# Performance work log

Hardware: AMD Instinct MI355X
Metric: run time of the kernel (lower is better)

Reference implementation:

```python
import jax, jax.numpy as jnp
from jax import lax
import numpy as np

B = 1024
CH = 32          # decomp.channel
LEVEL = 3        # decomp.level
CTOT = CH * (LEVEL + 1)   # 128, ODE state dim == GRU input dim
T_POINTS = 96    # decomp.eval_time_points
PRED_LEN = 96
HID = 128


def _dopri5_traj(y0, ts, Wo, bo):
    """Fixed-grid Dormand-Prince 5(4) integration of dy/dt = tanh(y Wo^T + bo).
    y0: [B, CTOT]; ts: [T]. Returns trajectory [T, B, CTOT]."""
    f = lambda y: jnp.tanh(y @ Wo.T + bo)

    def step(y, dt):
        k1 = f(y)
        k2 = f(y + dt * (0.2 * k1))
        k3 = f(y + dt * (3.0 / 40 * k1 + 9.0 / 40 * k2))
        k4 = f(y + dt * (44.0 / 45 * k1 - 56.0 / 15 * k2 + 32.0 / 9 * k3))
        k5 = f(y + dt * (19372.0 / 6561 * k1 - 25360.0 / 2187 * k2 + 64448.0 / 6561 * k3 - 212.0 / 729 * k4))
        k6 = f(y + dt * (9017.0 / 3168 * k1 - 355.0 / 33 * k2 + 46732.0 / 5247 * k3 + 49.0 / 176 * k4 - 5103.0 / 18656 * k5))
        y_next = y + dt * (35.0 / 384 * k1 + 500.0 / 1113 * k3 + 125.0 / 192 * k4 - 2187.0 / 6784 * k5 + 11.0 / 84 * k6)
        return y_next, y_next

    _, ys = lax.scan(step, y0, ts[1:] - ts[:-1])
    return jnp.concatenate([y0[None], ys], axis=0)


def _gru_layer(xs, W_ih, W_hh, b_ih, b_hh):
    """PyTorch-semantics GRU layer. xs: [T, B, D] -> hidden states [T, B, H]."""
    gi = jnp.einsum('tbd,gd->tbg', xs, W_ih) + b_ih  # precompute input gates
    H = W_hh.shape[1]

    def cell(h, gi_t):
        gh = h @ W_hh.T + b_hh
        i_r, i_z, i_n = jnp.split(gi_t, 3, axis=-1)
        h_r, h_z, h_n = jnp.split(gh, 3, axis=-1)
        r = jax.nn.sigmoid(i_r + h_r)
        z = jax.nn.sigmoid(i_z + h_z)
        n = jnp.tanh(i_n + r * h_n)
        h_new = (1.0 - z) * n + z * h
        return h_new, h_new

    h0 = jnp.zeros((xs.shape[1], H), xs.dtype)
    _, hs = lax.scan(cell, h0, gi)
    return hs


def setup_inputs() -> dict:
    key = jax.random.key(0)
    ks = jax.random.split(key, 20)
    s = 0.08  # ~1/sqrt(128), keeps GRU/ODE in a stable regime
    return {
        'x': jax.random.normal(ks[0], (B, CH, 256), jnp.float32),
        'yl': jax.random.normal(ks[1], (B, CH, 1), jnp.float32),
        'yh': jax.random.normal(ks[2], (B, CH * LEVEL, 1), jnp.float32),
        'W_ode': jax.random.normal(ks[3], (CTOT, CTOT), jnp.float32) * 0.05,
        'b_ode': jax.random.normal(ks[4], (CTOT,), jnp.float32) * 0.05,
        'W_ih0': jax.random.normal(ks[5], (3 * HID, CTOT), jnp.float32) * s,
        'W_hh0': jax.random.normal(ks[6], (3 * HID, HID), jnp.float32) * s,
        'b_ih0': jax.random.normal(ks[7], (3 * HID,), jnp.float32) * s,
        'b_hh0': jax.random.normal(ks[8], (3 * HID,), jnp.float32) * s,
        'W_ih1': jax.random.normal(ks[9], (3 * HID, HID), jnp.float32) * s,
        'W_hh1': jax.random.normal(ks[10], (3 * HID, HID), jnp.float32) * s,
        'b_ih1': jax.random.normal(ks[11], (3 * HID,), jnp.float32) * s,
        'b_hh1': jax.random.normal(ks[12], (3 * HID,), jnp.float32) * s,
        'W1': jax.random.normal(ks[13], (64, HID), jnp.float32) * s,
        'b1': jax.random.normal(ks[14], (64,), jnp.float32) * s,
        'W2': jax.random.normal(ks[15], (PRED_LEN * CH, 64), jnp.float32) * 0.125,
        'b2': jax.random.normal(ks[16], (PRED_LEN * CH,), jnp.float32) * 0.125,
    }


def reference(x, yl, yh, W_ode, b_ode,
              W_ih0, W_hh0, b_ih0, b_hh0,
              W_ih1, W_hh1, b_ih1, b_hh1,
              W1, b1, W2, b2):
    # coeffs = cat([yl] + yh, dim=1) -> [B, CTOT, 1] -> squeeze coeff length (=1)
    coeffs = jnp.concatenate([yl, yh], axis=1)[..., 0]  # [B, CTOT]
    ts = jnp.linspace(0.0, 1.0, T_POINTS)
    traj = _dopri5_traj(coeffs, ts, W_ode, b_ode)  # [T, B, CTOT]
    # rearrange 't b c l -> b t (c l)' with l == 1; GRU scans over leading T axis
    h1 = _gru_layer(traj, W_ih0, W_hh0, b_ih0, b_hh0)   # [T, B, HID]
    h2 = _gru_layer(h1, W_ih1, W_hh1, b_ih1, b_hh1)     # [T, B, HID]
    last = h2[-1]                                        # [B, HID]
    hidden = jax.nn.gelu(last @ W1.T + b1, approximate=False)
    pred = hidden @ W2.T + b2                            # [B, PRED_LEN*CH]
    return pred.reshape(-1, CH, PRED_LEN)
```

## Files before the change

kernel.cpp:

```cpp
#include <hip/hip_runtime.h>
#include <hip/hip_bf16.h>
#include <math.h>

#define TPTS 96
#define CTOT 128
#define LDP 134

typedef __bf16 bf16x8_t __attribute__((ext_vector_type(8)));
typedef float f32x4_t __attribute__((ext_vector_type(4)));
typedef unsigned short us8_t __attribute__((ext_vector_type(8)));

__device__ __forceinline__ unsigned short f2b(float f) {
    union { float f; unsigned int i; } v; v.f = f;
    unsigned int r = v.i + 0x7fffu + ((v.i >> 16) & 1u);
    return (unsigned short)(r >> 16);
}
__device__ __forceinline__ unsigned int packbf2(float a, float b) {
    return (unsigned int)f2b(a) | ((unsigned int)f2b(b) << 16);
}
__device__ __forceinline__ uint2 pack4(float v0, float v1, float v2, float v3) {
    uint2 w; w.x = packbf2(v0, v1); w.y = packbf2(v2, v3); return w;
}
__device__ __forceinline__ f32x4_t mfma16(bf16x8_t a, bf16x8_t b, f32x4_t c) {
    return __builtin_amdgcn_mfma_f32_16x16x32_bf16(a, b, c, 0, 0, 0);
}
__device__ __forceinline__ bf16x8_t ldfrag(const unsigned short* p) {
    us8_t v = *(const us8_t*)p;
    return __builtin_bit_cast(bf16x8_t, v);
}
__device__ __forceinline__ bf16x8_t ldfragW(const float* p) {
    float4 a = *(const float4*)p;
    float4 b = *(const float4*)(p + 4);
    bf16x8_t r;
    r[0] = __builtin_bit_cast(__bf16, f2b(a.x)); r[1] = __builtin_bit_cast(__bf16, f2b(a.y));
    r[2] = __builtin_bit_cast(__bf16, f2b(a.z)); r[3] = __builtin_bit_cast(__bf16, f2b(a.w));
    r[4] = __builtin_bit_cast(__bf16, f2b(b.x)); r[5] = __builtin_bit_cast(__bf16, f2b(b.y));
    r[6] = __builtin_bit_cast(__bf16, f2b(b.z)); r[7] = __builtin_bit_cast(__bf16, f2b(b.w));
    return r;
}
__device__ __forceinline__ float tanh2(float x) {
    float e = __expf(x + x);
    return 1.f - __fdividef(2.f, e + 1.f);
}
__device__ __forceinline__ float sigm(float x) {
    return __fdividef(1.f, 1.f + __expf(-x));
}

__device__ __forceinline__ void waitflag(unsigned int* f, unsigned int want) {
    if (threadIdx.x == 0) {
        int guard = 0;
        while (__hip_atomic_load(f, __ATOMIC_ACQUIRE, __HIP_MEMORY_SCOPE_AGENT) != want) {
            __builtin_amdgcn_s_sleep(2);
            if (++guard > (1 << 21)) break;
        }
    }
    __syncthreads();
}
__device__ __forceinline__ void setflag(unsigned int* f, unsigned int val) {
    if (threadIdx.x == 0)
        __hip_atomic_store(f, val, __ATOMIC_RELEASE, __HIP_MEMORY_SCOPE_AGENT);
}

__global__ void __launch_bounds__(512, 2)
ode_forecaster(const float* __restrict__ yl,
               const float* __restrict__ yh,
               const float* __restrict__ Wode,
               const float* __restrict__ bode,
               const float* __restrict__ Wih0,
               const float* __restrict__ Whh0,
               const float* __restrict__ bih0,
               const float* __restrict__ bhh0,
               const float* __restrict__ Wih1,
               const float* __restrict__ Whh1,
               const float* __restrict__ bih1,
               const float* __restrict__ bhh1,
               const float* __restrict__ W1v,
               const float* __restrict__ b1v,
               const float* __restrict__ W2v,
               const float* __restrict__ b2v,
               float* __restrict__ outp,
               char* __restrict__ wsb)
{
    const int role = blockIdx.x >> 6;
    const int c    = blockIdx.x & 63;
    const int tid  = threadIdx.x, lane = tid & 63, wv = tid >> 6;
    const int l15  = lane & 15, quad = lane >> 4;
    const int fbase = wv * 16 + quad * 4;
    const int rbase = c * 16;

    __shared__ __align__(16) unsigned short zbuf[2][16][LDP];
    __shared__ __align__(16) unsigned short hidbuf[16][72];

    unsigned short* yTraj  = (unsigned short*)(wsb);
    unsigned short* h1Traj = (unsigned short*)(wsb + 0x2000000);
    unsigned int*   yflag  = (unsigned int*)(wsb + 0x4000000);
    unsigned int*   h1flag = (unsigned int*)(wsb + 0x4010000);
#define YMAGIC(t)  (0x5E000000u + (unsigned)(t))
#define H1MAGIC(t) (0x6E000000u + (unsigned)(t))

    if (role == 0) {
        bf16x8_t wode[4];
#pragma unroll
        for (int kt = 0; kt < 4; ++kt)
            wode[kt] = ldfragW(Wode + (wv * 16 + l15) * CTOT + kt * 32 + quad * 8);
        float bo[4];
        {
            float4 b4 = *(const float4*)(bode + fbase);
            bo[0] = b4.x; bo[1] = b4.y; bo[2] = b4.z; bo[3] = b4.w;
        }
        float y[4];
        {
            int row = rbase + l15;
#pragma unroll
            for (int i = 0; i < 4; ++i) {
                int f = fbase + i;
                y[i] = (f < 32) ? yl[row * 32 + f] : yh[row * 96 + (f - 32)];
            }
            uint2 pk = pack4(y[0], y[1], y[2], y[3]);
            *(uint2*)&zbuf[0][l15][fbase] = pk;
            *(uint2*)(yTraj + ((size_t)row) * CTOT + fbase) = pk;
        }
        __syncthreads();
        setflag(&yflag[c * 128 + 0], YMAGIC(0));

        const float dt = 1.0f / 95.0f;
        const float d10 = dt * 0.2f;
        const float d20 = dt * (3.f/40.f),  d21 = dt * (9.f/40.f);
        const float d30 = dt * (44.f/45.f), d31 = dt * (-56.f/15.f), d32 = dt * (32.f/9.f);
        const float d40 = dt * (19372.f/6561.f), d41 = dt * (-25360.f/2187.f),
                    d42 = dt * (64448.f/6561.f), d43 = dt * (-212.f/729.f);
        const float d50 = dt * (9017.f/3168.f), d51 = dt * (-355.f/33.f),
                    d52 = dt * (46732.f/5247.f), d53 = dt * (49.f/176.f),
                    d54 = dt * (-5103.f/18656.f);
        const float e0 = dt * (35.f/384.f), e2 = dt * (500.f/1113.f), e3 = dt * (125.f/192.f),
                    e4 = dt * (-2187.f/6784.f), e5 = dt * (11.f/84.f);

        int p = 0;
        float kr[6][4];
#pragma unroll 1
        for (int t = 0; t < 95; ++t) {
#pragma unroll
            for (int s = 0; s < 6; ++s) {
                bf16x8_t bf[4];
#pragma unroll
                for (int kt = 0; kt < 4; ++kt)
                    bf[kt] = ldfrag(&zbuf[p][l15][kt * 32 + quad * 8]);
                f32x4_t a0 = {0.f, 0.f, 0.f, 0.f}, a1 = {0.f, 0.f, 0.f, 0.f};
                a0 = mfma16(wode[0], bf[0], a0);
                a1 = mfma16(wode[1], bf[1], a1);
                a0 = mfma16(wode[2], bf[2], a0);
                a1 = mfma16(wode[3], bf[3], a1);
                f32x4_t acc = a0 + a1;
#pragma unroll
                for (int i = 0; i < 4; ++i) kr[s][i] = tanh2(acc[i] + bo[i]);

                if (s < 5) {
                    float z[4];
#pragma unroll
                    for (int i = 0; i < 4; ++i) {
                        float zv;
                        if (s == 0)      zv = y[i] + d10 * kr[0][i];
                        else if (s == 1) zv = y[i] + d20 * kr[0][i] + d21 * kr[1][i];
                        else if (s == 2) zv = y[i] + d30 * kr[0][i] + d31 * kr[1][i] + d32 * kr[2][i];
                        else if (s == 3) zv = y[i] + d40 * kr[0][i] + d41 * kr[1][i]
                                             + d42 * kr[2][i] + d43 * kr[3][i];
                        else             zv = y[i] + d50 * kr[0][i] + d51 * kr[1][i]
                                             + d52 * kr[2][i] + d53 * kr[3][i] + d54 * kr[4][i];
                        z[i] = zv;
                    }
                    *(uint2*)&zbuf[p ^ 1][l15][fbase] = pack4(z[0], z[1], z[2], z[3]);
                } else {
#pragma unroll
                    for (int i = 0; i < 4; ++i)
                        y[i] += e0*kr[0][i] + e2*kr[2][i] + e3*kr[3][i] + e4*kr[4][i] + e5*kr[5][i];
                    uint2 pk = pack4(y[0], y[1], y[2], y[3]);
                    *(uint2*)&zbuf[p ^ 1][l15][fbase] = pk;
                    *(uint2*)(yTraj + ((size_t)(t + 1) * 1024 + rbase + l15) * CTOT + fbase) = pk;
                }
                __syncthreads();
                p ^= 1;
                if (s == 5) setflag(&yflag[c * 128 + t + 1], YMAGIC(t + 1));
            }
        }
        return;
    }

    const float* Wih = (role == 1) ? Wih0 : Wih1;
    const float* Whh = (role == 1) ? Whh0 : Whh1;
    const float* bih = (role == 1) ? bih0 : bih1;
    const float* bhh = (role == 1) ? bhh0 : bhh1;
    const unsigned short* src = (role == 1) ? yTraj : h1Traj;
    unsigned int* sflag = (role == 1) ? yflag : h1flag;

    bf16x8_t wih[3][4], whh[3][4];
#pragma unroll
    for (int g = 0; g < 3; ++g)
#pragma unroll
        for (int kt = 0; kt < 4; ++kt) {
            wih[g][kt] = ldfragW(Wih + (size_t)(g * 128 + wv * 16 + l15) * CTOT + kt * 32 + quad * 8);
            whh[g][kt] = ldfragW(Whh + (size_t)(g * 128 + wv * 16 + l15) * CTOT + kt * 32 + quad * 8);
        }
    float br[4], bz[4], bin_[4], bhn[4];
    {
        float4 a0 = *(const float4*)(bih + 0 * 128 + fbase);
        float4 b0 = *(const float4*)(bhh + 0 * 128 + fbase);
        float4 a1 = *(const float4*)(bih + 1 * 128 + fbase);
        float4 b1 = *(const float4*)(bhh + 1 * 128 + fbase);
        float4 a2 = *(const float4*)(bih + 2 * 128 + fbase);
        float4 b2 = *(const float4*)(bhh + 2 * 128 + fbase);
        br[0] = a0.x + b0.x; br[1] = a0.y + b0.y; br[2] = a0.z + b0.z; br[3] = a0.w + b0.w;
        bz[0] = a1.x + b1.x; bz[1] = a1.y + b1.y; bz[2] = a1.z + b1.z; bz[3] = a1.w + b1.w;
        bin_[0] = a2.x; bin_[1] = a2.y; bin_[2] = a2.z; bin_[3] = a2.w;
        bhn[0] = b2.x; bhn[1] = b2.y; bhn[2] = b2.z; bhn[3] = b2.w;
    }

    float h[4] = {0.f, 0.f, 0.f, 0.f};
    *(uint2*)&zbuf[0][l15][fbase] = pack4(0.f, 0.f, 0.f, 0.f);
    int p = 0;
    __syncthreads();

#pragma unroll 1
    for (int t = 0; t < TPTS; ++t) {
        waitflag(&sflag[c * 128 + t], (role == 1) ? YMAGIC(t) : H1MAGIC(t));
        const unsigned short* xp = src + ((size_t)t * 1024 + rbase + l15) * CTOT;
        bf16x8_t ax[4], ah[4];
#pragma unroll
        for (int kt = 0; kt < 4; ++kt) {
            ax[kt] = ldfrag(xp + kt * 32 + quad * 8);
            ah[kt] = ldfrag(&zbuf[p][l15][kt * 32 + quad * 8]);
        }
        f32x4_t gx[3], gh[3];
#pragma unroll
        for (int g = 0; g < 3; ++g) {
            gx[g] = (f32x4_t){0.f, 0.f, 0.f, 0.f};
            gh[g] = (f32x4_t){0.f, 0.f, 0.f, 0.f};
        }
#pragma unroll
        for (int kt = 0; kt < 4; ++kt) {
            gx[0] = mfma16(wih[0][kt], ax[kt], gx[0]);
            gx[1] = mfma16(wih[1][kt], ax[kt], gx[1]);
            gx[2] = mfma16(wih[2][kt], ax[kt], gx[2]);
            gh[0] = mfma16(whh[0][kt], ah[kt], gh[0]);
            gh[1] = mfma16(whh[1][kt], ah[kt], gh[1]);
            gh[2] = mfma16(whh[2][kt], ah[kt], gh[2]);
        }
#pragma unroll
        for (int i = 0; i < 4; ++i) {
            float rr = sigm(gx[0][i] + gh[0][i] + br[i]);
            float zz = sigm(gx[1][i] + gh[1][i] + bz[i]);
            float nn = tanh2((gx[2][i] + bin_[i]) + rr * (gh[2][i] + bhn[i]));
            h[i] = nn + zz * (h[i] - nn);
        }
        uint2 pk = pack4(h[0], h[1], h[2], h[3]);
        *(uint2*)&zbuf[p ^ 1][l15][fbase] = pk;
        if (role == 1)
            *(uint2*)(h1Traj + ((size_t)t * 1024 + rbase + l15) * CTOT + fbase) = pk;
        __syncthreads();
        if (role == 1) setflag(&h1flag[c * 128 + t], H1MAGIC(t));
        p ^= 1;
    }
    if (role == 1) return;

    if (wv < 4) {
        bf16x8_t wf[4], hf[4];
#pragma unroll
        for (int kt = 0; kt < 4; ++kt) {
            wf[kt] = ldfragW(W1v + (size_t)(wv * 16 + l15) * CTOT + kt * 32 + quad * 8);
            hf[kt] = ldfrag(&zbuf[p][l15][kt * 32 + quad * 8]);
        }
        f32x4_t acc = {0.f, 0.f, 0.f, 0.f};
#pragma unroll
        for (int kt = 0; kt < 4; ++kt) acc = mfma16(wf[kt], hf[kt], acc);
        float4 bb = *(const float4*)(b1v + wv * 16 + quad * 4);
        const float* bbp = (const float*)&bb;
        float gl[4];
#pragma unroll
        for (int i = 0; i < 4; ++i) {
            float x = acc[i] + bbp[i];
            gl[i] = 0.5f * x * (1.0f + erff(x * 0.70710678118654752f));
        }
        *(uint2*)&hidbuf[l15][wv * 16 + quad * 4] = pack4(gl[0], gl[1], gl[2], gl[3]);
    }
    __syncthreads();

    bf16x8_t ahid[2];
#pragma unroll
    for (int kt = 0; kt < 2; ++kt)
        ahid[kt] = ldfrag(&hidbuf[l15][kt * 32 + quad * 8]);
#pragma unroll 1
    for (int j = 0; j < 24; ++j) {
        int mt2 = wv * 24 + j;
        bf16x8_t wf0 = ldfragW(W2v + (size_t)(mt2 * 16 + l15) * 64 + quad * 8);
        bf16x8_t wf1 = ldfragW(W2v + (size_t)(mt2 * 16 + l15) * 64 + 32 + quad * 8);
        float4 bv = *(const float4*)(b2v + mt2 * 16 + quad * 4);
        const float* bvp = (const float*)&bv;
        f32x4_t acc = {0.f, 0.f, 0.f, 0.f};
        acc = mfma16(wf0, ahid[0], acc);
        acc = mfma16(wf1, ahid[1], acc);
        float4 o;
        o.x = acc[0] + bvp[0]; o.y = acc[1] + bvp[1];
        o.z = acc[2] + bvp[2]; o.w = acc[3] + bvp[3];
        *(float4*)(outp + (size_t)(rbase + l15) * 3072 + mt2 * 16 + quad * 4) = o;
    }
#undef YMAGIC
#undef H1MAGIC
}

extern "C" void kernel_launch(void* const* d_in, const int* in_sizes, int n_in,
                              void* d_out, int out_size, void* d_ws, size_t ws_size,
                              hipStream_t stream) {
    const float* yl   = (const float*)d_in[1];
    const float* yh   = (const float*)d_in[2];
    const float* Wode = (const float*)d_in[3];
    const float* bode = (const float*)d_in[4];
    const float* Wih0 = (const float*)d_in[5];
    const float* Whh0 = (const float*)d_in[6];
    const float* bih0 = (const float*)d_in[7];
    const float* bhh0 = (const float*)d_in[8];
    const float* Wih1 = (const float*)d_in[9];
    const float* Whh1 = (const float*)d_in[10];
    const float* bih1 = (const float*)d_in[11];
    const float* bhh1 = (const float*)d_in[12];
    const float* W1v  = (const float*)d_in[13];
    const float* b1v  = (const float*)d_in[14];
    const float* W2v  = (const float*)d_in[15];
    const float* b2v  = (const float*)d_in[16];

    ode_forecaster<<<dim3(192), dim3(512), 0, stream>>>(
        yl, yh, Wode, bode, Wih0, Whh0, bih0, bhh0,
        Wih1, Whh1, bih1, bhh1, W1v, b1v, W2v, b2v,
        (float*)d_out, (char*)d_ws);
}
```

Baseline: 798.2 us.

## Add dedicated communication wave for cross-block trajectory handoff with system-scope flags

Adds a ninth wavefront per block that copies each finished 16-row tile from LDS to the global trajectory buffer with system-scope relaxed atomic stores, drains the stores, then sets the ready flag. Compute waves no longer issue global stores or flag releases. Flag waits switch to relaxed system-scope loads with a shorter sleep. It also replaces the exp-based tanh with a clamped rational approximation and uses a hardware packed bf16 convert, trading some accuracy and relying on vmcnt draining rather than release semantics for ordering.

```diff
diff --git a/kernel.cpp b/kernel.cpp
--- a/kernel.cpp
+++ b/kernel.cpp
@@ -5,6 +5,7 @@
 #define TPTS 96
 #define CTOT 128
 #define LDP 134
+#define NTHR 576
 
 typedef __bf16 bf16x8_t __attribute__((ext_vector_type(8)));
 typedef float f32x4_t __attribute__((ext_vector_type(4)));
@@ -16,7 +17,13 @@
     return (unsigned short)(r >> 16);
 }
 __device__ __forceinline__ unsigned int packbf2(float a, float b) {
+#if __has_builtin(__builtin_amdgcn_cvt_pk_bf16_f32)
+    typedef __bf16 bf16x2_t __attribute__((ext_vector_type(2)));
+    bf16x2_t v = __builtin_amdgcn_cvt_pk_bf16_f32(a, b);
+    return __builtin_bit_cast(unsigned int, v);
+#else
     return (unsigned int)f2b(a) | ((unsigned int)f2b(b) << 16);
+#endif
 }
 __device__ __forceinline__ uint2 pack4(float v0, float v1, float v2, float v3) {
     uint2 w; w.x = packbf2(v0, v1); w.y = packbf2(v2, v3); return w;
@@ -38,30 +45,46 @@
     r[6] = __builtin_bit_cast(__bf16, f2b(b.z)); r[7] = __builtin_bit_cast(__bf16, f2b(b.w));
     return r;
 }
-__device__ __forceinline__ float tanh2(float x) {
-    float e = __expf(x + x);
-    return 1.f - __fdividef(2.f, e + 1.f);
+__device__ __forceinline__ float tanhp(float x) {
+    float xc = fminf(fmaxf(x, -4.5f), 4.5f);
+    float t = xc * xc;
+    float n = xc * (135135.f + t * (17325.f + t * (378.f + t)));
+    float d = 135135.f + t * (62370.f + t * (3150.f + 28.f * t));
+    return n * __frcp_rn(d);
 }
 __device__ __forceinline__ float sigm(float x) {
     return __fdividef(1.f, 1.f + __expf(-x));
 }
 
-__device__ __forceinline__ void waitflag(unsigned int* f, unsigned int want) {
+__device__ __forceinline__ void setflag_sys(unsigned int* f, unsigned int val) {
+    __hip_atomic_store(f, val, __ATOMIC_RELAXED, __HIP_MEMORY_SCOPE_SYSTEM);
+}
+__device__ __forceinline__ void waitflag_sys(unsigned int* f, unsigned int want) {
     if (threadIdx.x == 0) {
         int guard = 0;
-        while (__hip_atomic_load(f, __ATOMIC_ACQUIRE, __HIP_MEMORY_SCOPE_AGENT) != want) {
-            __builtin_amdgcn_s_sleep(2);
-            if (++guard > (1 << 21)) break;
+        while (__hip_atomic_load(f, __ATOMIC_RELAXED, __HIP_MEMORY_SCOPE_SYSTEM) != want) {
+            __builtin_amdgcn_s_sleep(1);
+            if (++guard > (1 << 22)) break;
         }
     }
     __syncthreads();
 }
-__device__ __forceinline__ void setflag(unsigned int* f, unsigned int val) {
-    if (threadIdx.x == 0)
-        __hip_atomic_store(f, val, __ATOMIC_RELEASE, __HIP_MEMORY_SCOPE_AGENT);
-}
-
-__global__ void __launch_bounds__(512, 2)
+__device__ __forceinline__ void dma_rows16(const unsigned short zb[16][LDP],
+                                           unsigned long long* dst, int lane) {
+    const int quad = lane >> 4, l15 = lane & 15;
+#pragma unroll
+    for (int i = 0; i < 4; ++i) {
+        int row = i * 4 + quad;
+        us8_t v = *(const us8_t*)&zb[row][l15 * 8];
+        union { us8_t v; unsigned long long q[2]; } u; u.v = v;
+        size_t idx = (size_t)row * 32 + l15 * 2;
+        __hip_atomic_store(dst + idx,     u.q[0], __ATOMIC_RELAXED, __HIP_MEMORY_SCOPE_SYSTEM);
+        __hip_atomic_store(dst + idx + 1, u.q[1], __ATOMIC_RELAXED, __HIP_MEMORY_SCOPE_SYSTEM);
+    }
+}
+#define DRAIN() asm volatile("s_waitcnt vmcnt(0)" ::: "memory")
+
+__global__ void __launch_bounds__(NTHR, 1)
 ode_forecaster(const float* __restrict__ yl,
                const float* __restrict__ yh,
                const float* __restrict__ Wode,
@@ -85,7 +108,7 @@
     const int c    = blockIdx.x & 63;
     const int tid  = threadIdx.x, lane = tid & 63, wv = tid >> 6;
     const int l15  = lane & 15, quad = lane >> 4;
-    const int fbase = wv * 16 + quad * 4;
+    const int fbase = (wv & 7) * 16 + quad * 4;
     const int rbase = c * 16;
 
     __shared__ __align__(16) unsigned short zbuf[2][16][LDP];
@@ -100,28 +123,27 @@
 
     if (role == 0) {
         bf16x8_t wode[4];
-#pragma unroll
-        for (int kt = 0; kt < 4; ++kt)
-            wode[kt] = ldfragW(Wode + (wv * 16 + l15) * CTOT + kt * 32 + quad * 8);
-        float bo[4];
-        {
+        float bo[4], y[4], kr[6][4];
+        if (wv < 8) {
+#pragma unroll
+            for (int kt = 0; kt < 4; ++kt)
+                wode[kt] = ldfragW(Wode + (wv * 16 + l15) * CTOT + kt * 32 + quad * 8);
             float4 b4 = *(const float4*)(bode + fbase);
             bo[0] = b4.x; bo[1] = b4.y; bo[2] = b4.z; bo[3] = b4.w;
-        }
-        float y[4];
-        {
             int row = rbase + l15;
 #pragma unroll
             for (int i = 0; i < 4; ++i) {
                 int f = fbase + i;
                 y[i] = (f < 32) ? yl[row * 32 + f] : yh[row * 96 + (f - 32)];
             }
-            uint2 pk = pack4(y[0], y[1], y[2], y[3]);
-            *(uint2*)&zbuf[0][l15][fbase] = pk;
-            *(uint2*)(yTraj + ((size_t)row) * CTOT + fbase) = pk;
+            *(uint2*)&zbuf[0][l15][fbase] = pack4(y[0], y[1], y[2], y[3]);
         }
         __syncthreads();
-        setflag(&yflag[c * 128 + 0], YMAGIC(0));
+        if (wv == 8) {
+            dma_rows16(zbuf[0], (unsigned long long*)(yTraj + (size_t)rbase * CTOT), lane);
+            DRAIN();
+            setflag_sys(&yflag[c * 128 + 0], YMAGIC(0));
+        }
 
         const float dt = 1.0f / 95.0f;
         const float d10 = dt * 0.2f;
@@ -136,50 +158,55 @@
                     e4 = dt * (-2187.f/6784.f), e5 = dt * (11.f/84.f);
 
         int p = 0;
-        float kr[6][4];
 #pragma unroll 1
         for (int t = 0; t < 95; ++t) {
 #pragma unroll
             for (int s = 0; s < 6; ++s) {
-                bf16x8_t bf[4];
-#pragma unroll
-                for (int kt = 0; kt < 4; ++kt)
-                    bf[kt] = ldfrag(&zbuf[p][l15][kt * 32 + quad * 8]);
-                f32x4_t a0 = {0.f, 0.f, 0.f, 0.f}, a1 = {0.f, 0.f, 0.f, 0.f};
-                a0 = mfma16(wode[0], bf[0], a0);
-                a1 = mfma16(wode[1], bf[1], a1);
-                a0 = mfma16(wode[2], bf[2], a0);
-                a1 = mfma16(wode[3], bf[3], a1);
-                f32x4_t acc = a0 + a1;
-#pragma unroll
-                for (int i = 0; i < 4; ++i) kr[s][i] = tanh2(acc[i] + bo[i]);
-
-                if (s < 5) {
-                    float z[4];
-#pragma unroll
-                    for (int i = 0; i < 4; ++i) {
-                        float zv;
-                        if (s == 0)      zv = y[i] + d10 * kr[0][i];
-                        else if (s == 1) zv = y[i] + d20 * kr[0][i] + d21 * kr[1][i];
-                        else if (s == 2) zv = y[i] + d30 * kr[0][i] + d31 * kr[1][i] + d32 * kr[2][i];
-                        else if (s == 3) zv = y[i] + d40 * kr[0][i] + d41 * kr[1][i]
-                                             + d42 * kr[2][i] + d43 * kr[3][i];
-                        else             zv = y[i] + d50 * kr[0][i] + d51 * kr[1][i]
-                                             + d52 * kr[2][i] + d53 * kr[3][i] + d54 * kr[4][i];
-                        z[i] = zv;
+                if (wv < 8) {
+                    bf16x8_t bf[4];
+#pragma unroll
+                    for (int kt = 0; kt < 4; ++kt)
+                        bf[kt] = ldfrag(&zbuf[p][l15][kt * 32 + quad * 8]);
+                    f32x4_t a0 = {0.f, 0.f, 0.f, 0.f}, a1 = {0.f, 0.f, 0.f, 0.f};
+                    a0 = mfma16(wode[0], bf[0], a0);
+                    a1 = mfma16(wode[1], bf[1], a1);
+                    a0 = mfma16(wode[2], bf[2], a0);
+                    a1 = mfma16(wode[3], bf[3], a1);
+                    f32x4_t acc = a0 + a1;
+#pragma unroll
+                    for (int i = 0; i < 4; ++i) kr[s][i] = tanhp(acc[i] + bo[i]);
+
+                    if (s < 5) {
+                        float z[4];
+#pragma unroll
+                        for (int i = 0; i < 4; ++i) {
+                            float zv;
+                            if (s == 0)      zv = y[i] + d10 * kr[0][i];
+                            else if (s == 1) zv = y[i] + d20 * kr[0][i] + d21 * kr[1][i];
+                            else if (s == 2) zv = y[i] + d30 * kr[0][i] + d31 * kr[1][i] + d32 * kr[2][i];
+                            else if (s == 3) zv = y[i] + d40 * kr[0][i] + d41 * kr[1][i]
+                                                 + d42 * kr[2][i] + d43 * kr[3][i];
+                            else             zv = y[i] + d50 * kr[0][i] + d51 * kr[1][i]
+                                                 + d52 * kr[2][i] + d53 * kr[3][i] + d54 * kr[4][i];
+                            z[i] = zv;
+                        }
+                        *(uint2*)&zbuf[p ^ 1][l15][fbase] = pack4(z[0], z[1], z[2], z[3]);
+                    } else {
+#pragma unroll
+                        for (int i = 0; i < 4; ++i)
+                            y[i] += e0*kr[0][i] + e2*kr[2][i] + e3*kr[3][i] + e4*kr[4][i] + e5*kr[5][i];
+                        *(uint2*)&zbuf[p ^ 1][l15][fbase] = pack4(y[0], y[1], y[2], y[3]);
                     }
-                    *(uint2*)&zbuf[p ^ 1][l15][fbase] = pack4(z[0], z[1], z[2], z[3]);
-                } else {
-#pragma unroll
-                    for (int i = 0; i < 4; ++i)
-                        y[i] += e0*kr[0][i] + e2*kr[2][i] + e3*kr[3][i] + e4*kr[4][i] + e5*kr[5][i];
-                    uint2 pk = pack4(y[0], y[1], y[2], y[3]);
-                    *(uint2*)&zbuf[p ^ 1][l15][fbase] = pk;
-                    *(uint2*)(yTraj + ((size_t)(t + 1) * 1024 + rbase + l15) * CTOT + fbase) = pk;
                 }
                 __syncthreads();
                 p ^= 1;
-                if (s == 5) setflag(&yflag[c * 128 + t + 1], YMAGIC(t + 1));
+                if (wv == 8 && s == 5) {
+                    dma_rows16(zbuf[p],
+                        (unsigned long long*)(yTraj + ((size_t)(t + 1) * 1024 + rbase) * CTOT),
+                        lane);
+                    DRAIN();
+                    setflag_sys(&yflag[c * 128 + t + 1], YMAGIC(t + 1));
+                }
             }
         }
         return;
@@ -193,15 +220,16 @@
     unsigned int* sflag = (role == 1) ? yflag : h1flag;
 
     bf16x8_t wih[3][4], whh[3][4];
-#pragma unroll
-    for (int g = 0; g < 3; ++g)
-#pragma unroll
-        for (int kt = 0; kt < 4; ++kt) {
-            wih[g][kt] = ldfragW(Wih + (size_t)(g * 128 + wv * 16 + l15) * CTOT + kt * 32 + quad * 8);
-            whh[g][kt] = ldfragW(Whh + (size_t)(g * 128 + wv * 16 + l15) * CTOT + kt * 32 + quad * 8);
-        }
     float br[4], bz[4], bin_[4], bhn[4];
-    {
+    float h[4] = {0.f, 0.f, 0.f, 0.f};
+    if (wv < 8) {
+#pragma unroll
+        for (int g = 0; g < 3; ++g)
+#pragma unroll
+            for (int kt = 0; kt < 4; ++kt) {
+                wih[g][kt] = ldfragW(Wih + (size_t)(g * 128 + wv * 16 + l15) * CTOT + kt * 32 + quad * 8);
+                whh[g][kt] = ldfragW(Whh + (size_t)(g * 128 + wv * 16 + l15) * CTOT + kt * 32 + quad * 8);
+            }
         float4 a0 = *(const float4*)(bih + 0 * 128 + fbase);
         float4 b0 = *(const float4*)(bhh + 0 * 128 + fbase);
         float4 a1 = *(const float4*)(bih + 1 * 128 + fbase);
@@ -212,51 +240,53 @@
         bz[0] = a1.x + b1.x; bz[1] = a1.y + b1.y; bz[2] = a1.z + b1.z; bz[3] = a1.w + b1.w;
         bin_[0] = a2.x; bin_[1] = a2.y; bin_[2] = a2.z; bin_[3] = a2.w;
         bhn[0] = b2.x; bhn[1] = b2.y; bhn[2] = b2.z; bhn[3] = b2.w;
-    }
-
-    float h[4] = {0.f, 0.f, 0.f, 0.f};
-    *(uint2*)&zbuf[0][l15][fbase] = pack4(0.f, 0.f, 0.f, 0.f);
+        *(uint2*)&zbuf[0][l15][fbase] = pack4(0.f, 0.f, 0.f, 0.f);
+    }
     int p = 0;
     __syncthreads();
 
 #pragma unroll 1
     for (int t = 0; t < TPTS; ++t) {
-        waitflag(&sflag[c * 128 + t], (role == 1) ? YMAGIC(t) : H1MAGIC(t));
-        const unsigned short* xp = src + ((size_t)t * 1024 + rbase + l15) * CTOT;
-        bf16x8_t ax[4], ah[4];
-#pragma unroll
-        for (int kt = 0; kt < 4; ++kt) {
-            ax[kt] = ldfrag(xp + kt * 32 + quad * 8);
-            ah[kt] = ldfrag(&zbuf[p][l15][kt * 32 + quad * 8]);
-        }
-        f32x4_t gx[3], gh[3];
-#pragma unroll
-        for (int g = 0; g < 3; ++g) {
-            gx[g] = (f32x4_t){0.f, 0.f, 0.f, 0.f};
-            gh[g] = (f32x4_t){0.f, 0.f, 0.f, 0.f};
-        }
-#pragma unroll
-        for (int kt = 0; kt < 4; ++kt) {
-            gx[0] = mfma16(wih[0][kt], ax[kt], gx[0]);
-            gx[1] = mfma16(wih[1][kt], ax[kt], gx[1]);
-            gx[2] = mfma16(wih[2][kt], ax[kt], gx[2]);
-            gh[0] = mfma16(whh[0][kt], ah[kt], gh[0]);
-            gh[1] = mfma16(whh[1][kt], ah[kt], gh[1]);
-            gh[2] = mfma16(whh[2][kt], ah[kt], gh[2]);
-        }
-#pragma unroll
-        for (int i = 0; i < 4; ++i) {
-            float rr = sigm(gx[0][i] + gh[0][i] + br[i]);
-            float zz = sigm(gx[1][i] + gh[1][i] + bz[i]);
-            float nn = tanh2((gx[2][i] + bin_[i]) + rr * (gh[2][i] + bhn[i]));
-            h[i] = nn + zz * (h[i] - nn);
-        }
-        uint2 pk = pack4(h[0], h[1], h[2], h[3]);
-        *(uint2*)&zbuf[p ^ 1][l15][fbase] = pk;
-        if (role == 1)
-            *(uint2*)(h1Traj + ((size_t)t * 1024 + rbase + l15) * CTOT + fbase) = pk;
+        waitflag_sys(&sflag[c * 128 + t], (role == 1) ? YMAGIC(t) : H1MAGIC(t));
+        if (wv < 8) {
+            const unsigned short* xp = src + ((size_t)t * 1024 + rbase + l15) * CTOT;
+            bf16x8_t ax[4], ah[4];
+#pragma unroll
+            for (int kt = 0; kt < 4; ++kt) {
+                ax[kt] = ldfrag(xp + kt * 32 + quad * 8);
+                ah[kt] = ldfrag(&zbuf[p][l15][kt * 32 + quad * 8]);
+            }
+            f32x4_t gx[3], gh[3];
+#pragma unroll
+            for (int g = 0; g < 3; ++g) {
+                gx[g] = (f32x4_t){0.f, 0.f, 0.f, 0.f};
+                gh[g] = (f32x4_t){0.f, 0.f, 0.f, 0.f};
+            }
+#pragma unroll
+            for (int kt = 0; kt < 4; ++kt) {
+                gx[0] = mfma16(wih[0][kt], ax[kt], gx[0]);
+                gx[1] = mfma16(wih[1][kt], ax[kt], gx[1]);
+                gx[2] = mfma16(wih[2][kt], ax[kt], gx[2]);
+                gh[0] = mfma16(whh[0][kt], ah[kt], gh[0]);
+                gh[1] = mfma16(whh[1][kt], ah[kt], gh[1]);
+                gh[2] = mfma16(whh[2][kt], ah[kt], gh[2]);
+            }
+#pragma unroll
+            for (int i = 0; i < 4; ++i) {
+                float rr = sigm(gx[0][i] + gh[0][i] + br[i]);
+                float zz = sigm(gx[1][i] + gh[1][i] + bz[i]);
+                float nn = tanhp((gx[2][i] + bin_[i]) + rr * (gh[2][i] + bhn[i]));
+                h[i] = nn + zz * (h[i] - nn);
+            }
+            *(uint2*)&zbuf[p ^ 1][l15][fbase] = pack4(h[0], h[1], h[2], h[3]);
+        }
         __syncthreads();
-        if (role == 1) setflag(&h1flag[c * 128 + t], H1MAGIC(t));
+        if (role == 1 && wv == 8) {
+            dma_rows16(zbuf[p ^ 1],
+                (unsigned long long*)(h1Traj + ((size_t)t * 1024 + rbase) * CTOT), lane);
+            DRAIN();
+            setflag_sys(&h1flag[c * 128 + t], H1MAGIC(t));
+        }
         p ^= 1;
     }
     if (role == 1) return;
@@ -282,25 +312,26 @@
         *(uint2*)&hidbuf[l15][wv * 16 + quad * 4] = pack4(gl[0], gl[1], gl[2], gl[3]);
     }
     __syncthreads();
-
-    bf16x8_t ahid[2];
-#pragma unroll
-    for (int kt = 0; kt < 2; ++kt)
-        ahid[kt] = ldfrag(&hidbuf[l15][kt * 32 + quad * 8]);
+    if (wv < 8) {
+        bf16x8_t ahid[2];
+#pragma unroll
+        for (int kt = 0; kt < 2; ++kt)
+            ahid[kt] = ldfrag(&hidbuf[l15][kt * 32 + quad * 8]);
 #pragma unroll 1
-    for (int j = 0; j < 24; ++j) {
-        int mt2 = wv * 24 + j;
-        bf16x8_t wf0 = ldfragW(W2v + (size_t)(mt2 * 16 + l15) * 64 + quad * 8);
-        bf16x8_t wf1 = ldfragW(W2v + (size_t)(mt2 * 16 + l15) * 64 + 32 + quad * 8);
-        float4 bv = *(const float4*)(b2v + mt2 * 16 + quad * 4);
-        const float* bvp = (const float*)&bv;
-        f32x4_t acc = {0.f, 0.f, 0.f, 0.f};
-        acc = mfma16(wf0, ahid[0], acc);
-        acc = mfma16(wf1, ahid[1], acc);
-        float4 o;
-        o.x = acc[0] + bvp[0]; o.y = acc[1] + bvp[1];
-        o.z = acc[2] + bvp[2]; o.w = acc[3] + bvp[3];
-        *(float4*)(outp + (size_t)(rbase + l15) * 3072 + mt2 * 16 + quad * 4) = o;
+        for (int j = 0; j < 24; ++j) {
+            int mt2 = wv * 24 + j;
+            bf16x8_t wf0 = ldfragW(W2v + (size_t)(mt2 * 16 + l15) * 64 + quad * 8);
+            bf16x8_t wf1 = ldfragW(W2v + (size_t)(mt2 * 16 + l15) * 64 + 32 + quad * 8);
+            float4 bv = *(const float4*)(b2v + mt2 * 16 + quad * 4);
+            const float* bvp = (const float*)&bv;
+            f32x4_t acc = {0.f, 0.f, 0.f, 0.f};
+            acc = mfma16(wf0, ahid[0], acc);
+            acc = mfma16(wf1, ahid[1], acc);
+            float4 o;
+            o.x = acc[0] + bvp[0]; o.y = acc[1] + bvp[1];
+            o.z = acc[2] + bvp[2]; o.w = acc[3] + bvp[3];
+            *(float4*)(outp + (size_t)(rbase + l15) * 3072 + mt2 * 16 + quad * 4) = o;
+        }
     }
 #undef YMAGIC
 #undef H1MAGIC
@@ -326,7 +357,7 @@
     const float* W2v  = (const float*)d_in[15];
     const float* b2v  = (const float*)d_in[16];
 
-    ode_forecaster<<<dim3(192), dim3(512), 0, stream>>>(
+    ode_forecaster<<<dim3(192), dim3(NTHR), 0, stream>>>(
         yl, yh, Wode, bode, Wih0, Whh0, bih0, bhh0,
         Wih1, Whh1, bih1, bhh1, W1v, b1v, W2v, b2v,
         (float*)d_out, (char*)d_ws);
```

Result: no change. 806.5 us (+1.0%).
